# Performance work log

Measured on AMD Instinct MI355X. Metric: run time of the kernel, lower is better.

Reference implementation:

```python
import jax, jax.numpy as jnp
import numpy as np

N_NODES = 50000
N_EDGES = 800000
NODE_DIM = 3
EDGE_DIM = 32
HIDDEN = 128
NUM_GRAPHS = 256


def _linear_init(key, fan_in, fan_out):
    # torch nn.Linear default: U(-1/sqrt(fan_in), 1/sqrt(fan_in))
    kw, kb = jax.random.split(key)
    bound = 1.0 / np.sqrt(fan_in)
    W = jax.random.uniform(kw, (fan_in, fan_out), jnp.float32, -bound, bound)
    b = jax.random.uniform(kb, (fan_out,), jnp.float32, -bound, bound)
    return W, b


def setup_inputs() -> dict:
    key = jax.random.key(0)
    ks = jax.random.split(key, 16)
    x = jax.random.normal(ks[0], (N_NODES, NODE_DIM), jnp.float32)
    edge_index = jax.random.randint(ks[1], (2, N_EDGES), 0, N_NODES, jnp.int64)
    edge_attr = jax.random.uniform(ks[2], (N_EDGES, EDGE_DIM), jnp.float32)
    batch = jnp.sort(jax.random.randint(ks[3], (N_NODES,), 0, NUM_GRAPHS, jnp.int64))

    # conv1: CGConv(channels=3, dim=32) -> lin_f, lin_s: (2*3+32) -> 3
    Wf1, bf1 = _linear_init(ks[4], 2 * NODE_DIM + EDGE_DIM, NODE_DIM)
    Ws1, bs1 = _linear_init(ks[5], 2 * NODE_DIM + EDGE_DIM, NODE_DIM)
    # node_proj: 3 -> 128
    Wp, bp = _linear_init(ks[6], NODE_DIM, HIDDEN)
    zin = 2 * HIDDEN + EDGE_DIM
    Wf_list, bf_list, Ws_list, bs_list = [], [], [], []
    for i in range(2):
        Wf, bf = _linear_init(ks[7 + i], zin, HIDDEN)
        Ws, bs = _linear_init(ks[9 + i], zin, HIDDEN)
        Wf_list.append(Wf); bf_list.append(bf); Ws_list.append(Ws); bs_list.append(bs)
    Wf_convs = jnp.stack(Wf_list); bf_convs = jnp.stack(bf_list)
    Ws_convs = jnp.stack(Ws_list); bs_convs = jnp.stack(bs_list)
    # fc1: 128 -> 128
    W1, b1 = _linear_init(ks[11], HIDDEN, HIDDEN)
    # 5 heads: 128 -> 1, stacked as (5, 128) and (5,)
    Wh_list, bh_list = [], []
    for i in range(5):
        Wh, bh = _linear_init(jax.random.fold_in(ks[12], i), HIDDEN, 1)
        Wh_list.append(Wh[:, 0]); bh_list.append(bh[0])
    W_heads = jnp.stack(Wh_list)  # (5, 128)
    b_heads = jnp.stack(bh_list)  # (5,)

    return dict(x=x, edge_index=edge_index, edge_attr=edge_attr, batch=batch,
                Wf1=Wf1, bf1=bf1, Ws1=Ws1, bs1=bs1, Wp=Wp, bp=bp,
                Wf_convs=Wf_convs, bf_convs=bf_convs, Ws_convs=Ws_convs, bs_convs=bs_convs,
                W1=W1, b1=b1, W_heads=W_heads, b_heads=b_heads)


def _cgconv(x, src, dst, edge_attr, Wf, bf, Ws, bs):
    # PyG CGConv: z_ij = [x_i || x_j || e_ij], messages aggregated to i (dst)
    z = jnp.concatenate([x[dst], x[src], edge_attr], axis=-1)  # [E, 2C+D]
    msg = jax.nn.sigmoid(z @ Wf + bf) * jax.nn.softplus(z @ Ws + bs)  # [E, C]
    agg = jax.ops.segment_sum(msg, dst, num_segments=x.shape[0])
    return x + agg


def reference(x, edge_index, edge_attr, batch,
              Wf1, bf1, Ws1, bs1, Wp, bp,
              Wf_convs, bf_convs, Ws_convs, bs_convs,
              W1, b1, W_heads, b_heads):
    src, dst = edge_index[0], edge_index[1]
    h = _cgconv(x, src, dst, edge_attr, Wf1, bf1, Ws1, bs1)
    h = jax.nn.relu(h @ Wp + bp)
    for l in range(Wf_convs.shape[0]):
        h = _cgconv(h, src, dst, edge_attr, Wf_convs[l], bf_convs[l], Ws_convs[l], bs_convs[l])
        h = jax.nn.relu(h)
    # global mean pool over graphs
    sums = jax.ops.segment_sum(h, batch, num_segments=NUM_GRAPHS)
    counts = jax.ops.segment_sum(jnp.ones((h.shape[0],), h.dtype), batch, num_segments=NUM_GRAPHS)
    g = sums / jnp.maximum(counts, 1.0)[:, None]  # [G, H]
    g = jax.nn.relu(g @ W1 + b1)
    # 5 heads stacked -> [G, 5] (columns: volume, band_gap, formation_energy, density, bulk_modulus)
    out = g @ W_heads.T + b_heads
    return out
```

## Files before the change

kernel.cpp:

```cpp
#include <hip/hip_runtime.h>
#include <hip/hip_bf16.h>
#include <math.h>

#define N_NODES 50000
#define N_EDGES 800000
#define NODE_DIM 3
#define EDGE_DIM 32
#define HIDDEN 128
#define NUM_GRAPHS 256
#define ZIN (2*HIDDEN + EDGE_DIM)
#define NPAD 50176

#define LOG2E 1.44269504088896f
#define LN2   0.69314718055995f

typedef __attribute__((ext_vector_type(8))) short short8;
typedef __attribute__((ext_vector_type(4))) float f32x4;

__device__ __forceinline__ unsigned short f2bf(float x) {
    unsigned u = __float_as_uint(x);
    u += 0x7FFFu + ((u >> 16) & 1u);
    return (unsigned short)(u >> 16);
}
__device__ __forceinline__ float bf_lo(unsigned u) { return __uint_as_float(u << 16); }
__device__ __forceinline__ float bf_hi(unsigned u) { return __uint_as_float(u & 0xFFFF0000u); }

__global__ __launch_bounds__(256) void conv1_sorted_kernel(
    const float* __restrict__ x, const float* __restrict__ EA,
    const int4* __restrict__ epack,
    const float* __restrict__ Wf1, const float* __restrict__ bf1,
    const float* __restrict__ Ws1, const float* __restrict__ bs1,
    float* __restrict__ agg0)
{
    __shared__ float WfL[38*3], WsL[38*3], bfL[3], bsL[3];
    __shared__ float msgL[256*4];
    __shared__ int   pdL[256];

    if (threadIdx.x < 114) {
        WfL[threadIdx.x] = Wf1[threadIdx.x] * LOG2E;
        WsL[threadIdx.x] = Ws1[threadIdx.x] * LOG2E;
    }
    if (threadIdx.x < 3) {
        bfL[threadIdx.x] = bf1[threadIdx.x] * LOG2E;
        bsL[threadIdx.x] = bs1[threadIdx.x] * LOG2E;
    }
    __syncthreads();

    const int p = blockIdx.x * 256 + threadIdx.x;
    int4 e = epack[p];
    const int eid = e.x, s = e.y, d = e.z;
    pdL[threadIdx.x] = d;

    float z[38];
    z[0] = x[d*3+0]; z[1] = x[d*3+1]; z[2] = x[d*3+2];
    z[3] = x[s*3+0]; z[4] = x[s*3+1]; z[5] = x[s*3+2];
    const float4* ep = (const float4*)(EA + (size_t)eid * EDGE_DIM);
    #pragma unroll
    for (int q = 0; q < 8; ++q) {
        float4 v = ep[q];
        z[6+4*q+0] = v.x; z[6+4*q+1] = v.y; z[6+4*q+2] = v.z; z[6+4*q+3] = v.w;
    }
    float f[3], g[3];
    #pragma unroll
    for (int c = 0; c < 3; ++c) { f[c] = bfL[c]; g[c] = bsL[c]; }
    #pragma unroll
    for (int j = 0; j < 38; ++j) {
        #pragma unroll
        for (int c = 0; c < 3; ++c) {
            f[c] += z[j] * WfL[j*3+c];
            g[c] += z[j] * WsL[j*3+c];
        }
    }
    #pragma unroll
    for (int c = 0; c < 3; ++c) {
        float sig = __builtin_amdgcn_rcpf(1.0f + __builtin_amdgcn_exp2f(-f[c]));
        float sp  = __builtin_amdgcn_logf(1.0f + __builtin_amdgcn_exp2f(g[c]));
        msgL[threadIdx.x*4 + c] = sig * sp;
    }
    __syncthreads();

    if (threadIdx.x < 48) {
        const int c   = threadIdx.x % 3;
        const int seg = threadIdx.x / 3;
        const int base = seg * 16;
        float acc = 0.0f;
        int cur = pdL[base];
        #pragma unroll 4
        for (int i = 0; i < 16; ++i) {
            int dd = pdL[base + i];
            float v = msgL[(base + i)*4 + c];
            if (dd != cur) {
                atomicAdd(agg0 + (size_t)cur*3 + c, acc);
                acc = 0.0f; cur = dd;
            }
            acc += v;
        }
        atomicAdd(agg0 + (size_t)cur*3 + c, acc);
    }
}

__global__ __launch_bounds__(256) void proj_kernel(
    const float* __restrict__ x, const float* __restrict__ agg0,
    const float* __restrict__ Wp, const float* __restrict__ bp,
    float* __restrict__ H)
{
    int idx = blockIdx.x * 256 + threadIdx.x;
    if (idx >= N_NODES * HIDDEN) return;
    int n = idx >> 7, c = idx & 127;
    float h0 = fmaf(agg0[n*3+0], LN2, x[n*3+0]);
    float h1 = fmaf(agg0[n*3+1], LN2, x[n*3+1]);
    float h2 = fmaf(agg0[n*3+2], LN2, x[n*3+2]);
    float v = bp[c] + h0*Wp[0*128+c] + h1*Wp[1*128+c] + h2*Wp[2*128+c];
    H[idx] = fmaxf(v, 0.0f);
}

__global__ __launch_bounds__(256) void hist_kernel(
    const int* __restrict__ ei, int* __restrict__ hist)
{
    int e = blockIdx.x * 256 + threadIdx.x;
    if (e < N_EDGES) atomicAdd(&hist[ei[N_EDGES + e]], 1);
}

__global__ __launch_bounds__(256) void scanA_kernel(
    const int* __restrict__ hist, int* __restrict__ cursor, int* __restrict__ btot)
{
    __shared__ int tmp[256];
    int t = threadIdx.x;
    int i = blockIdx.x * 256 + t;
    int v = hist[i];
    tmp[t] = v;
    __syncthreads();
    #pragma unroll
    for (int off = 1; off < 256; off <<= 1) {
        int y = (t >= off) ? tmp[t - off] : 0;
        __syncthreads();
        if (t >= off) tmp[t] += y;
        __syncthreads();
    }
    cursor[i] = tmp[t] - v;
    if (t == 255) btot[blockIdx.x] = tmp[t];
}

__global__ __launch_bounds__(256) void scanB_kernel(int* __restrict__ btot)
{
    __shared__ int tmp[256];
    int t = threadIdx.x;
    int v = btot[t];
    tmp[t] = v;
    __syncthreads();
    #pragma unroll
    for (int off = 1; off < 256; off <<= 1) {
        int y = (t >= off) ? tmp[t - off] : 0;
        __syncthreads();
        if (t >= off) tmp[t] += y;
        __syncthreads();
    }
    btot[t] = tmp[t] - v;
}

__global__ __launch_bounds__(256) void scanC_kernel(
    int* __restrict__ cursor, const int* __restrict__ btot)
{
    int i = blockIdx.x * 256 + threadIdx.x;
    cursor[i] += btot[blockIdx.x];
}

__global__ __launch_bounds__(256) void scatter_kernel(
    const int* __restrict__ ei, int* __restrict__ cursor,
    int4* __restrict__ epack)
{
    int e = blockIdx.x * 256 + threadIdx.x;
    if (e >= N_EDGES) return;
    int s = ei[e];
    int d = ei[N_EDGES + e];
    int p = atomicAdd(&cursor[d], 1);
    epack[p] = make_int4(e, s, d, 0);
}

__global__ __launch_bounds__(256) void repack_frag_kernel(
    const float* __restrict__ Wf, const float* __restrict__ Ws,
    unsigned short* __restrict__ Bfrag)
{
    int idx = blockIdx.x * 256 + threadIdx.x;
    if (idx >= 2*32*4*64) return;
    int lane = idx & 63;
    int kc   = (idx >> 6) & 3;
    int nt   = (idx >> 8) & 31;
    int l    = idx >> 13;
    const float* wf  = Wf + (size_t)l * ZIN * HIDDEN;
    const float* wsp = Ws + (size_t)l * ZIN * HIDDEN;
    int n = nt*16 + (lane & 15);
    int half = n >> 8;
    int within = n & 255;
    int cc = within >> 1;
    int t = within & 1;
    const float* W = t ? wsp : wf;
    unsigned short vals[8];
    #pragma unroll
    for (int j = 0; j < 8; ++j) {
        int k = kc*32 + (lane >> 4)*8 + j;
        vals[j] = f2bf(W[(size_t)(half*128 + k)*128 + cc] * LOG2E);
    }
    *(short8*)(Bfrag + (size_t)idx * 8) = *(short8*)vals;
}

__global__ __launch_bounds__(256) void repack_edge_frag_kernel(
    const float* __restrict__ Wf, const float* __restrict__ Ws,
    unsigned short* __restrict__ BE)
{
    int idx = blockIdx.x * 256 + threadIdx.x;
    if (idx >= 2*16*64) return;
    int lane = idx & 63;
    int nt   = (idx >> 6) & 15;
    int l    = idx >> 10;
    const float* W = ((nt & 8) ? Ws : Wf) + (size_t)l * ZIN * HIDDEN + 256*128;
    int c = (nt & 7)*16 + (lane & 15);
    unsigned short vals[8];
    #pragma unroll
    for (int j = 0; j < 8; ++j) {
        int k = (lane >> 4)*8 + j;
        vals[j] = f2bf(W[(size_t)k*128 + c] * LOG2E);
    }
    *(short8*)(BE + (size_t)idx * 8) = *(short8*)vals;
}

__global__ __launch_bounds__(256) void gemm_mfma(
    const float* __restrict__ H, const float* __restrict__ aggIn,
    const unsigned short* __restrict__ Bfrag,
    const float* __restrict__ bf, const float* __restrict__ bs,
    unsigned short* __restrict__ Pb)
{
    const int lane = threadIdx.x & 63;
    const int wave = threadIdx.x >> 6;
    const int m    = lane & 15;
    const int quad = lane >> 4;
    const int rowA = blockIdx.y * 64 + wave * 16 + m;
    const int colBase = blockIdx.x * 256;

    const float* hrow = H + (size_t)rowA * 128;
    short8 a[4];
    #pragma unroll
    for (int kc = 0; kc < 4; ++kc) {
        float4 v0 = *(const float4*)(hrow + kc*32 + quad*8);
        float4 v1 = *(const float4*)(hrow + kc*32 + quad*8 + 4);
        if (aggIn) {
            const float* arow = aggIn + (size_t)rowA * 128;
            float4 a0 = *(const float4*)(arow + kc*32 + quad*8);
            float4 a1 = *(const float4*)(arow + kc*32 + quad*8 + 4);
        v0.x = fmaxf(fmaf(a0.x, LN2, v0.x), 0.f); v0.y = fmaxf(fmaf(a0.y, LN2, v0.y), 0.f);
        v0.z = fmaxf(fmaf(a0.z, LN2, v0.z), 0.f); v0.w = fmaxf(fmaf(a0.w, LN2, v0.w), 0.f);
        v1.x = fmaxf(fmaf(a1.x, LN2, v1.x), 0.f); v1.y = fmaxf(fmaf(a1.y, LN2, v1.y), 0.f);
        v1.z = fmaxf(fmaf(a1.z, LN2, v1.z), 0.f); v1.w = fmaxf(fmaf(a1.w, LN2, v1.w), 0.f);
        }
        unsigned short t[8];
        t[0]=f2bf(v0.x); t[1]=f2bf(v0.y); t[2]=f2bf(v0.z); t[3]=f2bf(v0.w);
        t[4]=f2bf(v1.x); t[5]=f2bf(v1.y); t[6]=f2bf(v1.z); t[7]=f2bf(v1.w);
        a[kc] = *(short8*)t;
    }

    f32x4 acc[16];
    #pragma unroll
    for (int nt = 0; nt < 16; ++nt) {
        float bias = 0.0f;
        if (colBase == 0) {
            int col = nt*16 + m;
            bias = ((col & 1) ? bs[col >> 1] : bf[col >> 1]) * LOG2E;
        }
        acc[nt] = (f32x4){bias, bias, bias, bias};
    }

    #pragma unroll
    for (int nt = 0; nt < 16; ++nt) {
        int ntg = (colBase >> 4) + nt;
        const unsigned short* bp = Bfrag + ((size_t)(ntg*4) * 64 + lane) * 8;
        #pragma unroll
        for (int kc = 0; kc < 4; ++kc) {
            short8 b = *(const short8*)(bp + (size_t)kc * 64 * 8);
            acc[nt] = __builtin_amdgcn_mfma_f32_16x16x32_bf16(a[kc], b, acc[nt], 0, 0, 0);
        }
    }

    const int rowC = blockIdx.y * 64 + wave * 16 + quad * 4;
    #pragma unroll
    for (int nt = 0; nt < 16; ++nt) {
        int col = colBase + nt*16 + m;
        #pragma unroll
        for (int r = 0; r < 4; ++r) {
            int row = rowC + r;
            if (row < N_NODES) Pb[(size_t)row * 512 + col] = f2bf(acc[nt][r]);
        }
    }
}

__global__ __launch_bounds__(256, 8) void edge_kernel(
    const unsigned short* __restrict__ Pb, const float* __restrict__ EA,
    const int4* __restrict__ epack,
    const unsigned short* __restrict__ BE,
    float* __restrict__ agg)
{
    __shared__ float msgL[64*68];
    __shared__ int pdL[64];
    __shared__ unsigned bmaskL[2];

    if (threadIdx.x < 64) {
        const int t = threadIdx.x;
        int d = epack[blockIdx.x*64 + t].z;
        pdL[t] = d;
        bool b = (t & 15) ? (d != pdL[t-1]) : false;
        unsigned long long bal = __ballot(b);
        if (t == 0) { bmaskL[0] = (unsigned)bal; bmaskL[1] = (unsigned)(bal >> 32); }
    }

    const int lane = threadIdx.x & 63;
    const int wave = threadIdx.x >> 6;
    const int m    = lane & 15;
    const int quad = lane >> 4;
    const int p0   = blockIdx.x * 64 + wave * 16;

    int eid = epack[p0 + m].x;
    const float* ea = EA + (size_t)eid * EDGE_DIM + quad*8;
    float4 v0 = *(const float4*)ea;
    float4 v1 = *(const float4*)(ea + 4);
    unsigned short t[8];
    t[0]=f2bf(v0.x); t[1]=f2bf(v0.y); t[2]=f2bf(v0.z); t[3]=f2bf(v0.w);
    t[4]=f2bf(v1.x); t[5]=f2bf(v1.y); t[6]=f2bf(v1.z); t[7]=f2bf(v1.w);
    short8 a = *(short8*)t;

    const unsigned short* pdp[4];
    const unsigned short* psp[4];
    #pragma unroll
    for (int r = 0; r < 4; ++r) {
        int4 e = epack[p0 + quad*4 + r];
        pdp[r] = Pb + (size_t)e.z * 512 + 2*m;
        psp[r] = Pb + (size_t)e.y * 512 + 256 + 2*m;
    }

    const short8* BEv = (const short8*)BE;
    const int chunk  = wave*4 + quad;
    const int c2  = threadIdx.x & 63;
    const int seg = threadIdx.x >> 6;

    #pragma unroll
    for (int half = 0; half < 2; ++half) {
        #pragma unroll
        for (int nt4 = 0; nt4 < 4; ++nt4) {
            const int nt = half*4 + nt4;
            short8 bF = BEv[nt*64 + lane];
            short8 bS = BEv[(nt+8)*64 + lane];
            f32x4 accF, accS;
            #pragma unroll
            for (int r = 0; r < 4; ++r) {
                unsigned pd = *(const unsigned*)(pdp[r] + nt*32);
                unsigned ps = *(const unsigned*)(psp[r] + nt*32);
                accF[r] = bf_lo(pd) + bf_lo(ps);
                accS[r] = bf_hi(pd) + bf_hi(ps);
            }
            f32x4 qf = __builtin_amdgcn_mfma_f32_16x16x32_bf16(a, bF, accF, 0, 0, 0);
            f32x4 qs = __builtin_amdgcn_mfma_f32_16x16x32_bf16(a, bS, accS, 0, 0, 0);
            float4 mv;
            #pragma unroll
            for (int r = 0; r < 4; ++r) {
                float sig = __builtin_amdgcn_rcpf(1.0f + __builtin_amdgcn_exp2f(-qf[r]));
                float sp  = __builtin_amdgcn_logf(1.0f + __builtin_amdgcn_exp2f(qs[r]));
                ((float*)&mv)[r] = sig * sp;
            }
            const int row = nt4*16 + m;
            const int chunkp = (chunk + 2*m) & 15;
            *(float4*)&msgL[row*68 + chunkp*4] = mv;
        }
        __syncthreads();

        unsigned mfull = bmaskL[seg >> 1];
        unsigned msk = (unsigned)__builtin_amdgcn_readfirstlane(
            (int)((mfull >> ((seg & 1) * 16)) & 0xFFFEu));
        const int swz = 2*(c2 & 15);
        const float* rowp = &msgL[c2*68];
        float* aggc = agg + half*64 + c2;
        const int base = seg*16;
        float acc = 0.0f;
        #pragma unroll
        for (int jj = 0; jj < 4; ++jj) {
            const int ch = seg*4 + jj;
            const float4 v4 = *(const float4*)&rowp[((ch + swz) & 15)*4];
            #pragma unroll
            for (int k = 0; k < 4; ++k) {
                if (msk & 1u) {
                    atomicAdd(&aggc[(size_t)pdL[base + jj*4 + k - 1] * HIDDEN], acc);
                    acc = 0.0f;
                }
                msk >>= 1;
                acc += ((const float*)&v4)[k];
            }
        }
        atomicAdd(&aggc[(size_t)pdL[base + 15] * HIDDEN], acc);
        if (half == 0) __syncthreads();
    }
}

__global__ __launch_bounds__(128) void pool_kernel(
    const float* __restrict__ H, const float* __restrict__ agg1,
    const float* __restrict__ agg2, const int* __restrict__ batch,
    float* __restrict__ gsum, float* __restrict__ gcnt)
{
    const int c = threadIdx.x;
    const int n0 = blockIdx.x * 128;
    float acc = 0.0f;
    int cur = -1;
    for (int i = 0; i < 128; ++i) {
        int n = n0 + i;
        if (n >= N_NODES) break;
        int g = batch[n];
        if (g != cur) {
            if (cur >= 0) atomicAdd(gsum + (size_t)cur * HIDDEN + c, acc);
            cur = g; acc = 0.0f;
        }
        size_t ix = (size_t)n * HIDDEN + c;
        float h = fmaxf(fmaf(agg2[ix], LN2, fmaxf(fmaf(agg1[ix], LN2, H[ix]), 0.0f)), 0.0f);
        acc += h;
    }
    if (cur >= 0) atomicAdd(gsum + (size_t)cur * HIDDEN + c, acc);

    if (c == 0) {
        int curg = -1; float run = 0.0f;
        for (int i = 0; i < 128; ++i) {
            int n = n0 + i;
            if (n >= N_NODES) break;
            int g = batch[n];
            if (g != curg) {
                if (curg >= 0) atomicAdd(gcnt + curg, run);
                curg = g; run = 0.0f;
            }
            run += 1.0f;
        }
        if (curg >= 0) atomicAdd(gcnt + curg, run);
    }
}

__global__ __launch_bounds__(128) void head_kernel(
    const float* __restrict__ gsum, const float* __restrict__ gcnt,
    const float* __restrict__ W1, const float* __restrict__ b1,
    const float* __restrict__ Wh, const float* __restrict__ bh,
    float* __restrict__ out)
{
    __shared__ float gavg[128];
    __shared__ float g1[128];
    const int g = blockIdx.x, c = threadIdx.x;
    float cnt = fmaxf(gcnt[g], 1.0f);
    gavg[c] = gsum[(size_t)g * HIDDEN + c] / cnt;
    __syncthreads();
    float acc = b1[c];
    for (int k = 0; k < 128; ++k) acc += gavg[k] * W1[k*128 + c];
    g1[c] = fmaxf(acc, 0.0f);
    __syncthreads();
    if (c < 5) {
        float o = bh[c];
        for (int k = 0; k < 128; ++k) o += g1[k] * Wh[c*128 + k];
        out[(size_t)g * 5 + c] = o;
    }
}

extern "C" void kernel_launch(void* const* d_in, const int* in_sizes, int n_in,
                              void* d_out, int out_size, void* d_ws, size_t ws_size,
                              hipStream_t stream) {
    const float* x        = (const float*)d_in[0];
    const int*   ei       = (const int*)  d_in[1];
    const float* EA       = (const float*)d_in[2];
    const int*   batch    = (const int*)  d_in[3];
    const float* Wf1      = (const float*)d_in[4];
    const float* bf1      = (const float*)d_in[5];
    const float* Ws1      = (const float*)d_in[6];
    const float* bs1      = (const float*)d_in[7];
    const float* Wp       = (const float*)d_in[8];
    const float* bp       = (const float*)d_in[9];
    const float* Wf_convs = (const float*)d_in[10];
    const float* bf_convs = (const float*)d_in[11];
    const float* Ws_convs = (const float*)d_in[12];
    const float* bs_convs = (const float*)d_in[13];
    const float* W1       = (const float*)d_in[14];
    const float* b1       = (const float*)d_in[15];
    const float* W_heads  = (const float*)d_in[16];
    const float* b_heads  = (const float*)d_in[17];
    float* out = (float*)d_out;

    float* ws = (float*)d_ws;
    float* agg0 = ws + 0;
    float* H    = ws + 150016;
    unsigned short* Pb = (unsigned short*)(ws + 6550016);
    float* agg1 = ws + 19350016;
    float* agg2 = ws + 25750016;
    unsigned short* Bfrag = (unsigned short*)(ws + 32150016);
    unsigned short* BE    = (unsigned short*)(ws + 32215552);
    float* gsum = ws + 32223744;
    float* gcnt = ws + 32256512;
    int* hist   = (int*)(ws + 32257024);
    int* cursor = (int*)(ws + 32307200);
    int* btot   = (int*)(ws + 32357376);
    int4* epack = (int4*)(ws + 32357632);

    hipMemsetAsync(hist, 0, (size_t)(2*NPAD + 256) * sizeof(int), stream);
    hist_kernel<<<(N_EDGES + 255)/256, 256, 0, stream>>>(ei, hist);
    scanA_kernel<<<NPAD/256, 256, 0, stream>>>(hist, cursor, btot);
    scanB_kernel<<<1, 256, 0, stream>>>(btot);
    scanC_kernel<<<NPAD/256, 256, 0, stream>>>(cursor, btot);
    scatter_kernel<<<(N_EDGES + 255)/256, 256, 0, stream>>>(ei, cursor, epack);

    hipMemsetAsync(agg0, 0, (size_t)N_NODES * 3 * sizeof(float), stream);
    conv1_sorted_kernel<<<N_EDGES/256, 256, 0, stream>>>(x, EA, epack, Wf1, bf1, Ws1, bs1, agg0);
    proj_kernel<<<(N_NODES*HIDDEN + 255)/256, 256, 0, stream>>>(x, agg0, Wp, bp, H);
    repack_frag_kernel<<<(2*32*4*64 + 255)/256, 256, 0, stream>>>(Wf_convs, Ws_convs, Bfrag);
    repack_edge_frag_kernel<<<(2*16*64 + 255)/256, 256, 0, stream>>>(Wf_convs, Ws_convs, BE);

    hipMemsetAsync(agg1, 0, (size_t)2 * N_NODES * HIDDEN * sizeof(float), stream);

    dim3 ggrid(2, (N_NODES + 63)/64);
    gemm_mfma<<<ggrid, 256, 0, stream>>>(H, nullptr, Bfrag, bf_convs, bs_convs, Pb);
    edge_kernel<<<N_EDGES/64, 256, 0, stream>>>(Pb, EA, epack, BE, agg1);
    gemm_mfma<<<ggrid, 256, 0, stream>>>(H, agg1, Bfrag + (size_t)32*4*64*8,
                                         bf_convs + HIDDEN, bs_convs + HIDDEN, Pb);
    edge_kernel<<<N_EDGES/64, 256, 0, stream>>>(Pb, EA, epack, BE + (size_t)16*64*8, agg2);

    hipMemsetAsync(gsum, 0, (size_t)(NUM_GRAPHS * HIDDEN + NUM_GRAPHS) * sizeof(float), stream);
    pool_kernel<<<(N_NODES + 127)/128, 128, 0, stream>>>(H, agg1, agg2, batch, gsum, gcnt);
    head_kernel<<<NUM_GRAPHS, 128, 0, stream>>>(gsum, gcnt, W1, b1, W_heads, b_heads, out);
}
```

Baseline: 664.2 us.

## Fold scan fixup into scatter, merge repack kernels, plain-store interior segments

Result: faster. 616.2 us (-7.2%).

```diff
diff --git a/kernel.cpp b/kernel.cpp
--- a/kernel.cpp
+++ b/kernel.cpp
@@ -33,7 +33,7 @@
     float* __restrict__ agg0)
 {
     __shared__ float WfL[38*3], WsL[38*3], bfL[3], bsL[3];
-    __shared__ float msgL[256*4];
+    __shared__ float msgL[256*5];
     __shared__ int   pdL[256];
 
     if (threadIdx.x < 114) {
@@ -75,7 +75,7 @@
     for (int c = 0; c < 3; ++c) {
         float sig = __builtin_amdgcn_rcpf(1.0f + __builtin_amdgcn_exp2f(-f[c]));
         float sp  = __builtin_amdgcn_logf(1.0f + __builtin_amdgcn_exp2f(g[c]));
-        msgL[threadIdx.x*4 + c] = sig * sp;
+        msgL[threadIdx.x*5 + c] = sig * sp;
     }
     __syncthreads();
 
@@ -88,7 +88,7 @@
         #pragma unroll 4
         for (int i = 0; i < 16; ++i) {
             int dd = pdL[base + i];
-            float v = msgL[(base + i)*4 + c];
+            float v = msgL[(base + i)*5 + c];
             if (dd != cur) {
                 atomicAdd(agg0 + (size_t)cur*3 + c, acc);
                 acc = 0.0f; cur = dd;
@@ -158,70 +158,58 @@
     btot[t] = tmp[t] - v;
 }
 
-__global__ __launch_bounds__(256) void scanC_kernel(
-    int* __restrict__ cursor, const int* __restrict__ btot)
-{
-    int i = blockIdx.x * 256 + threadIdx.x;
-    cursor[i] += btot[blockIdx.x];
-}
-
 __global__ __launch_bounds__(256) void scatter_kernel(
     const int* __restrict__ ei, int* __restrict__ cursor,
-    int4* __restrict__ epack)
+    const int* __restrict__ btot, int4* __restrict__ epack)
 {
     int e = blockIdx.x * 256 + threadIdx.x;
     if (e >= N_EDGES) return;
     int s = ei[e];
     int d = ei[N_EDGES + e];
-    int p = atomicAdd(&cursor[d], 1);
+    int p = atomicAdd(&cursor[d], 1) + btot[d >> 8];
     epack[p] = make_int4(e, s, d, 0);
 }
 
-__global__ __launch_bounds__(256) void repack_frag_kernel(
+__global__ __launch_bounds__(256) void repack_all_kernel(
     const float* __restrict__ Wf, const float* __restrict__ Ws,
-    unsigned short* __restrict__ Bfrag)
+    unsigned short* __restrict__ Bfrag, unsigned short* __restrict__ BE)
 {
     int idx = blockIdx.x * 256 + threadIdx.x;
-    if (idx >= 2*32*4*64) return;
-    int lane = idx & 63;
-    int kc   = (idx >> 6) & 3;
-    int nt   = (idx >> 8) & 31;
-    int l    = idx >> 13;
-    const float* wf  = Wf + (size_t)l * ZIN * HIDDEN;
-    const float* wsp = Ws + (size_t)l * ZIN * HIDDEN;
-    int n = nt*16 + (lane & 15);
-    int half = n >> 8;
-    int within = n & 255;
-    int cc = within >> 1;
-    int t = within & 1;
-    const float* W = t ? wsp : wf;
-    unsigned short vals[8];
-    #pragma unroll
-    for (int j = 0; j < 8; ++j) {
-        int k = kc*32 + (lane >> 4)*8 + j;
-        vals[j] = f2bf(W[(size_t)(half*128 + k)*128 + cc] * LOG2E);
-    }
-    *(short8*)(Bfrag + (size_t)idx * 8) = *(short8*)vals;
-}
-
-__global__ __launch_bounds__(256) void repack_edge_frag_kernel(
-    const float* __restrict__ Wf, const float* __restrict__ Ws,
-    unsigned short* __restrict__ BE)
-{
-    int idx = blockIdx.x * 256 + threadIdx.x;
-    if (idx >= 2*16*64) return;
-    int lane = idx & 63;
-    int nt   = (idx >> 6) & 15;
-    int l    = idx >> 10;
-    const float* W = ((nt & 8) ? Ws : Wf) + (size_t)l * ZIN * HIDDEN + 256*128;
-    int c = (nt & 7)*16 + (lane & 15);
-    unsigned short vals[8];
-    #pragma unroll
-    for (int j = 0; j < 8; ++j) {
-        int k = (lane >> 4)*8 + j;
-        vals[j] = f2bf(W[(size_t)k*128 + c] * LOG2E);
-    }
-    *(short8*)(BE + (size_t)idx * 8) = *(short8*)vals;
+    if (idx < 2*32*4*64) {
+        int lane = idx & 63;
+        int kc   = (idx >> 6) & 3;
+        int nt   = (idx >> 8) & 31;
+        int l    = idx >> 13;
+        const float* wf  = Wf + (size_t)l * ZIN * HIDDEN;
+        const float* wsp = Ws + (size_t)l * ZIN * HIDDEN;
+        int n = nt*16 + (lane & 15);
+        int half = n >> 8;
+        int within = n & 255;
+        int cc = within >> 1;
+        int t = within & 1;
+        const float* W = t ? wsp : wf;
+        unsigned short vals[8];
+        #pragma unroll
+        for (int j = 0; j < 8; ++j) {
+            int k = kc*32 + (lane >> 4)*8 + j;
+            vals[j] = f2bf(W[(size_t)(half*128 + k)*128 + cc] * LOG2E);
+        }
+        *(short8*)(Bfrag + (size_t)idx * 8) = *(short8*)vals;
+    } else if (idx < 2*32*4*64 + 2*16*64) {
+        int i2 = idx - 2*32*4*64;
+        int lane = i2 & 63;
+        int nt   = (i2 >> 6) & 15;
+        int l    = i2 >> 10;
+        const float* W = ((nt & 8) ? Ws : Wf) + (size_t)l * ZIN * HIDDEN + 256*128;
+        int c = (nt & 7)*16 + (lane & 15);
+        unsigned short vals[8];
+        #pragma unroll
+        for (int j = 0; j < 8; ++j) {
+            int k = (lane >> 4)*8 + j;
+            vals[j] = f2bf(W[(size_t)k*128 + c] * LOG2E);
+        }
+        *(short8*)(BE + (size_t)i2 * 8) = *(short8*)vals;
+    }
 }
 
 __global__ __launch_bounds__(256) void gemm_mfma(
@@ -378,6 +366,7 @@
         float* aggc = agg + half*64 + c2;
         const int base = seg*16;
         float acc = 0.0f;
+        bool inside = false;
         #pragma unroll
         for (int jj = 0; jj < 4; ++jj) {
             const int ch = seg*4 + jj;
@@ -385,8 +374,9 @@
             #pragma unroll
             for (int k = 0; k < 4; ++k) {
                 if (msk & 1u) {
-                    atomicAdd(&aggc[(size_t)pdL[base + jj*4 + k - 1] * HIDDEN], acc);
-                    acc = 0.0f;
+                    float* dp = &aggc[(size_t)pdL[base + jj*4 + k - 1] * HIDDEN];
+                    if (inside) *dp = acc; else atomicAdd(dp, acc);
+                    acc = 0.0f; inside = true;
                 }
                 msk >>= 1;
                 acc += ((const float*)&v4)[k];
@@ -403,10 +393,10 @@
     float* __restrict__ gsum, float* __restrict__ gcnt)
 {
     const int c = threadIdx.x;
-    const int n0 = blockIdx.x * 128;
+    const int n0 = blockIdx.x * 32;
     float acc = 0.0f;
     int cur = -1;
-    for (int i = 0; i < 128; ++i) {
+    for (int i = 0; i < 32; ++i) {
         int n = n0 + i;
         if (n >= N_NODES) break;
         int g = batch[n];
@@ -422,7 +412,7 @@
 
     if (c == 0) {
         int curg = -1; float run = 0.0f;
-        for (int i = 0; i < 128; ++i) {
+        for (int i = 0; i < 32; ++i) {
             int n = n0 + i;
             if (n >= N_NODES) break;
             int g = batch[n];
@@ -497,18 +487,17 @@
     int* btot   = (int*)(ws + 32357376);
     int4* epack = (int4*)(ws + 32357632);
 
-    hipMemsetAsync(hist, 0, (size_t)(2*NPAD + 256) * sizeof(int), stream);
+    hipMemsetAsync(hist, 0, (size_t)NPAD * sizeof(int), stream);
     hist_kernel<<<(N_EDGES + 255)/256, 256, 0, stream>>>(ei, hist);
     scanA_kernel<<<NPAD/256, 256, 0, stream>>>(hist, cursor, btot);
     scanB_kernel<<<1, 256, 0, stream>>>(btot);
-    scanC_kernel<<<NPAD/256, 256, 0, stream>>>(cursor, btot);
-    scatter_kernel<<<(N_EDGES + 255)/256, 256, 0, stream>>>(ei, cursor, epack);
+    scatter_kernel<<<(N_EDGES + 255)/256, 256, 0, stream>>>(ei, cursor, btot, epack);
 
     hipMemsetAsync(agg0, 0, (size_t)N_NODES * 3 * sizeof(float), stream);
     conv1_sorted_kernel<<<N_EDGES/256, 256, 0, stream>>>(x, EA, epack, Wf1, bf1, Ws1, bs1, agg0);
     proj_kernel<<<(N_NODES*HIDDEN + 255)/256, 256, 0, stream>>>(x, agg0, Wp, bp, H);
-    repack_frag_kernel<<<(2*32*4*64 + 255)/256, 256, 0, stream>>>(Wf_convs, Ws_convs, Bfrag);
-    repack_edge_frag_kernel<<<(2*16*64 + 255)/256, 256, 0, stream>>>(Wf_convs, Ws_convs, BE);
+    repack_all_kernel<<<(2*32*4*64 + 2*16*64 + 255)/256, 256, 0, stream>>>(
+        Wf_convs, Ws_convs, Bfrag, BE);
 
     hipMemsetAsync(agg1, 0, (size_t)2 * N_NODES * HIDDEN * sizeof(float), stream);
 
@@ -520,6 +509,6 @@
     edge_kernel<<<N_EDGES/64, 256, 0, stream>>>(Pb, EA, epack, BE + (size_t)16*64*8, agg2);
 
     hipMemsetAsync(gsum, 0, (size_t)(NUM_GRAPHS * HIDDEN + NUM_GRAPHS) * sizeof(float), stream);
-    pool_kernel<<<(N_NODES + 127)/128, 128, 0, stream>>>(H, agg1, agg2, batch, gsum, gcnt);
+    pool_kernel<<<(N_NODES + 31)/32, 128, 0, stream>>>(H, agg1, agg2, batch, gsum, gcnt);
     head_kernel<<<NUM_GRAPHS, 128, 0, stream>>>(gsum, gcnt, W1, b1, W_heads, b_heads, out);
 }
```
